# Kernel tuning notes

Measured on AMD Instinct MI355X. Metric: run time of the kernel, lower is better.

Reference implementation:

```python
import jax, jax.numpy as jnp
import numpy as np

B, S, E = 4, 4096, 1024
H = 16
D = E // H  # head_dim = 64


def setup_inputs() -> dict:
    key = jax.random.key(0)
    kx, kk, kq, kv = jax.random.split(key, 4)
    scale = 1.0 / np.sqrt(E)
    return {
        "x": jax.random.normal(kx, (B, S, E), dtype=jnp.float32),
        # torch nn.Linear weight shape: [out_features, in_features] = [D, E]
        "Wk": jax.random.uniform(kk, (D, E), dtype=jnp.float32, minval=-scale, maxval=scale),
        "Wq": jax.random.uniform(kq, (D, E), dtype=jnp.float32, minval=-scale, maxval=scale),
        "Wv": jax.random.uniform(kv, (D, E), dtype=jnp.float32, minval=-scale, maxval=scale),
    }


def reference(x, Wk, Wq, Wv):
    # Projections: x @ W^T  -> [B, S, D]
    k = jnp.einsum('bse,de->bsd', x, Wk)
    q = jnp.einsum('bse,de->bsd', x, Wq)
    v = jnp.einsum('bse,de->bsd', x, Wv)
    # Scaled scores [B, S, S]
    scores = jnp.einsum('bqd,bkd->bqk', q, k) * (D ** -0.5)
    # Causal mask: position q attends to k <= q
    causal = jnp.tril(jnp.ones((S, S), dtype=bool))
    scores = jnp.where(causal, scores, -jnp.inf)
    attn = jax.nn.softmax(scores, axis=-1)
    # dropout omitted (eval mode / attn_pdrop=0)
    out = jnp.einsum('bqk,bkd->bqd', attn, v)
    return out
```

## Files before the change

kernel.cpp:

```cpp
#include <hip/hip_runtime.h>
#include <hip/hip_bf16.h>
#include <stdint.h>

#define BB 4
#define SS 4096
#define EE 1024
#define DD 64

typedef __attribute__((ext_vector_type(8))) short short8;
typedef __attribute__((ext_vector_type(4))) float f32x4;

__device__ inline uint32_t cvtpk(float lo, float hi) {
    uint32_t r;
    asm("v_cvt_pk_bf16_f32 %0, %1, %2" : "=v"(r) : "v"(lo), "v"(hi));
    return r;
}
__device__ inline float bf2f_lo(uint32_t u) {
    union { uint32_t u; float f; } v; v.u = u << 16; return v.f;
}
__device__ inline float bf2f_hi(uint32_t u) {
    union { uint32_t u; float f; } v; v.u = u & 0xFFFF0000u; return v.f;
}

#define GL16(g, l) __builtin_amdgcn_global_load_lds( \
    (const __attribute__((address_space(1))) void*)(g), \
    (__attribute__((address_space(3))) void*)(l), 16, 0, 0)

__global__ __launch_bounds__(256) void wconv_kernel(
    const float* __restrict__ Wq, const float* __restrict__ Wk,
    const float* __restrict__ Wv, ushort* __restrict__ Wb)
{
    int tid = blockIdx.x * 256 + threadIdx.x;
    int sel = tid >> 13;
    int off = (tid & 8191) * 8;
    const float* src = (sel == 0) ? Wq : ((sel == 1) ? Wk : Wv);
    float4 a = *reinterpret_cast<const float4*>(src + off);
    float4 b = *reinterpret_cast<const float4*>(src + off + 4);
    uint4 o;
    o.x = cvtpk(a.x, a.y); o.y = cvtpk(a.z, a.w);
    o.z = cvtpk(b.x, b.y); o.w = cvtpk(b.z, b.w);
    *reinterpret_cast<uint4*>(Wb + (size_t)sel * 65536 + off) = o;
}

__global__ __launch_bounds__(256) void proj_kernel(
    const float* __restrict__ x, const ushort* __restrict__ Wb,
    ushort* __restrict__ q_ws, ushort* __restrict__ k_ws, ushort* __restrict__ vT_ws)
{
    __shared__ __align__(16) char smem[3 * 40960];
    const int t = threadIdx.x;
    const int wid = t >> 6, lane = t & 63, g = lane >> 4, lr = lane & 15;
    const int m0 = blockIdx.x * 64;
    const int NT = EE / 64;

    f32x4 acc[3][4];
#pragma unroll
    for (int ni = 0; ni < 3; ++ni)
#pragma unroll
        for (int mi = 0; mi < 4; ++mi) acc[ni][mi] = (f32x4)(0.0f);

#define PSTAGE(KT, BUFI) do { \
    char* xb_ = smem + (BUFI) * 40960; \
    char* wb_ = xb_ + 16384; \
    int e0_ = (KT) * 64; \
    _Pragma("unroll") \
    for (int i = 0; i < 4; ++i) { \
        int v = i * 256 + t; int row = v >> 4, c = v & 15; \
        GL16(&x[(size_t)(m0 + row) * EE + e0_ + ((c ^ (row & 15)) << 2)], xb_ + v * 16); \
    } \
    _Pragma("unroll") \
    for (int i = 0; i < 6; ++i) { \
        int v = i * 256 + t; int row = v >> 3, u = v & 7; \
        GL16(&Wb[(size_t)row * EE + e0_ + ((u ^ (row & 7)) << 3)], wb_ + v * 16); \
    } \
} while (0)

    PSTAGE(0, 0); PSTAGE(1, 1); PSTAGE(2, 2);

    for (int kt = 0; kt < NT; ++kt) {
        asm volatile("s_waitcnt vmcnt(20)" ::: "memory");
        __builtin_amdgcn_s_barrier();
        __builtin_amdgcn_sched_barrier(0);

        const char* xb = smem + (kt % 3) * 40960;
        const char* wb = xb + 16384;

        short8 af[3][2], bf[4][2];
#pragma unroll
        for (int ni = 0; ni < 3; ++ni) {
            int row = wid * 48 + ni * 16 + lr;
#pragma unroll
            for (int kc = 0; kc < 2; ++kc)
                af[ni][kc] = *reinterpret_cast<const short8*>(
                    wb + row * 128 + (((kc * 4 + g) ^ (row & 7)) << 4));
        }
#pragma unroll
        for (int mi = 0; mi < 4; ++mi) {
            int row = mi * 16 + lr;
#pragma unroll
            for (int kc = 0; kc < 2; ++kc) {
                int s0_ = (kc * 8 + 2 * g) ^ lr;
                int s1_ = (kc * 8 + 2 * g + 1) ^ lr;
                f32x4 lo = *reinterpret_cast<const f32x4*>(xb + row * 256 + s0_ * 16);
                f32x4 hi = *reinterpret_cast<const f32x4*>(xb + row * 256 + s1_ * 16);
                union { short8 s; uint32_t u[4]; } p;
                p.u[0] = cvtpk(lo[0], lo[1]); p.u[1] = cvtpk(lo[2], lo[3]);
                p.u[2] = cvtpk(hi[0], hi[1]); p.u[3] = cvtpk(hi[2], hi[3]);
                bf[mi][kc] = p.s;
            }
        }
#pragma unroll
        for (int ni = 0; ni < 3; ++ni)
#pragma unroll
            for (int mi = 0; mi < 4; ++mi)
#pragma unroll
                for (int kc = 0; kc < 2; ++kc)
                    acc[ni][mi] = __builtin_amdgcn_mfma_f32_16x16x32_bf16(af[ni][kc], bf[mi][kc], acc[ni][mi], 0, 0, 0);

        asm volatile("s_waitcnt lgkmcnt(0)" ::: "memory");
        __builtin_amdgcn_sched_barrier(0);
        __builtin_amdgcn_s_barrier();
        __builtin_amdgcn_sched_barrier(0);

        int nx = (kt + 3 < NT) ? kt + 3 : NT - 1;
        PSTAGE(nx, kt % 3);
    }

    asm volatile("s_waitcnt vmcnt(0)" ::: "memory");

#pragma unroll
    for (int ni = 0; ni < 3; ++ni) {
        int n0 = wid * 48 + ni * 16 + 4 * g;
        int sel = n0 >> 6, d0 = n0 & 63;
#pragma unroll
        for (int mi = 0; mi < 4; ++mi) {
            int m = m0 + mi * 16 + lr;
            int b = m >> 12, s = m & (SS - 1);
            uint2 p;
            p.x = cvtpk(acc[ni][mi][0], acc[ni][mi][1]);
            p.y = cvtpk(acc[ni][mi][2], acc[ni][mi][3]);
            if (sel == 0) {
                *reinterpret_cast<uint2*>(q_ws + ((size_t)b * SS + s) * DD + d0) = p;
            } else if (sel == 1) {
                *reinterpret_cast<uint2*>(k_ws + ((size_t)b * SS + s) * DD + d0) = p;
            } else {
                vT_ws[((size_t)b * DD + d0 + 0) * SS + s] = (ushort)(p.x & 0xFFFF);
                vT_ws[((size_t)b * DD + d0 + 1) * SS + s] = (ushort)(p.x >> 16);
                vT_ws[((size_t)b * DD + d0 + 2) * SS + s] = (ushort)(p.y & 0xFFFF);
                vT_ws[((size_t)b * DD + d0 + 3) * SS + s] = (ushort)(p.y >> 16);
            }
        }
    }
}

__global__ __launch_bounds__(512) void attn_kernel(
    const ushort* __restrict__ q_ws, const ushort* __restrict__ k_ws,
    const ushort* __restrict__ vT_ws, uint32_t* __restrict__ pO32,
    float* __restrict__ pml)
{
    __shared__ __align__(16) char kv_lds[2][32768];
    const int t = threadIdx.x;
    const int wid = t >> 6, lane = t & 63, g = lane >> 4, lr = lane & 15;
    const int bid = blockIdx.x;
    const int f = bid & 3;
    const int b = (bid >> 2) & 3;
    const int qblk = 31 - (bid >> 4);
    const int qb_w = qblk * 128 + wid * 16;

    const ushort* qp = q_ws + ((size_t)b * SS + qb_w + lr) * DD;
    short8 qf0 = *reinterpret_cast<const short8*>(qp + g * 8);
    short8 qf1 = *reinterpret_cast<const short8*>(qp + 32 + g * 8);

    float l_r = 0.0f;
    f32x4 acc[4];
#pragma unroll
    for (int i = 0; i < 4; ++i) acc[i] = (f32x4)(0.0f);

    const float sc = 0.125f * 1.44269504f;
    const float MB = 5.770780164f;
    const int nt = qblk + 1;
    const int nfull = ((qb_w - 127) >> 7) + 1;
    const int cs = (nt + 3) >> 2;
    const int t0 = f * cs;
    const int t1 = min(nt, (f + 1) * cs);
    const ushort* kbase = k_ws + (size_t)b * SS * DD;
    const ushort* vbase = vT_ws + (size_t)b * DD * SS;

    const int s0 = g & 1, hi = g >> 1;
    const int idxA = ((lr + 16 * ((s0 << 1) | hi)) << 2);
    const int idxB = idxA ^ 128;

#define ASTAGE(KT, BUFI) do { \
    char* kb_ = kv_lds[BUFI]; \
    int kv0_ = (KT) * 128; \
    _Pragma("unroll") \
    for (int i = 0; i < 2; ++i) { \
        int v = i * 512 + t; int row = v >> 3, c = v & 7; \
        GL16(kbase + (size_t)(kv0_ + row) * DD + ((c ^ (row & 7)) << 3), kb_ + v * 16); \
    } \
    _Pragma("unroll") \
    for (int i = 0; i < 2; ++i) { \
        int v = i * 512 + t; int row = v >> 4, c = v & 15; \
        GL16(vbase + (size_t)row * SS + kv0_ + ((c ^ ((row & 7) << 1)) << 3), kb_ + 16384 + v * 16); \
    } \
} while (0)

    if (t0 < t1) {
        ASTAGE(t0, 0);
        ASTAGE((t0 + 1 < t1) ? t0 + 1 : t0, 1);

        for (int kt = t0; kt < t1; ++kt) {
            const int cur = (kt - t0) & 1;
            asm volatile("s_waitcnt vmcnt(4)" ::: "memory");
            __builtin_amdgcn_s_barrier();
            __builtin_amdgcn_sched_barrier(0);

            const char* kb = kv_lds[cur];
            const char* vb = kb + 16384;
            const int kv0 = kt * 128;

            f32x4 sfr[8];
            __builtin_amdgcn_s_setprio(1);
#pragma unroll
            for (int nf = 0; nf < 8; ++nf) {
                int row = nf * 16 + lr;
                short8 b0 = *reinterpret_cast<const short8*>(kb + row * 128 + ((g ^ (row & 7)) << 4));
                short8 b1 = *reinterpret_cast<const short8*>(kb + row * 128 + (((4 + g) ^ (row & 7)) << 4));
                f32x4 s_ = (f32x4)(0.0f);
                s_ = __builtin_amdgcn_mfma_f32_16x16x32_bf16(b0, qf0, s_, 0, 0, 0);
                s_ = __builtin_amdgcn_mfma_f32_16x16x32_bf16(b1, qf1, s_, 0, 0, 0);
                sfr[nf] = s_;
            }
            __builtin_amdgcn_s_setprio(0);

            if (kt >= nfull) {
#pragma unroll
                for (int nf = 0; nf < 8; ++nf)
#pragma unroll
                    for (int jr = 0; jr < 4; ++jr)
                        if (kv0 + nf * 16 + 4 * g + jr > qb_w + lr) sfr[nf][jr] = -1e30f;
            }

            float ps = 0.0f;
            uint32_t pk[16];
#pragma unroll
            for (int nf = 0; nf < 8; ++nf) {
                float e0_ = exp2f(fmaf(sfr[nf][0], sc, -MB));
                float e1_ = exp2f(fmaf(sfr[nf][1], sc, -MB));
                float e2_ = exp2f(fmaf(sfr[nf][2], sc, -MB));
                float e3_ = exp2f(fmaf(sfr[nf][3], sc, -MB));
                ps += (e0_ + e1_) + (e2_ + e3_);
                pk[nf * 2 + 0] = cvtpk(e0_, e1_);
                pk[nf * 2 + 1] = cvtpk(e2_, e3_);
            }
            l_r += ps;

            uint32_t pw[4][4];
#pragma unroll
            for (int cc = 0; cc < 4; ++cc) {
                uint32_t r0 = (uint32_t)__builtin_amdgcn_ds_permute(idxA, (int)(s0 ? pk[cc * 4 + 2] : pk[cc * 4 + 0]));
                uint32_t r1 = (uint32_t)__builtin_amdgcn_ds_permute(idxA, (int)(s0 ? pk[cc * 4 + 3] : pk[cc * 4 + 1]));
                uint32_t r2 = (uint32_t)__builtin_amdgcn_ds_permute(idxB, (int)(s0 ? pk[cc * 4 + 0] : pk[cc * 4 + 2]));
                uint32_t r3 = (uint32_t)__builtin_amdgcn_ds_permute(idxB, (int)(s0 ? pk[cc * 4 + 1] : pk[cc * 4 + 3]));
                pw[cc][0] = hi ? r2 : r0;
                pw[cc][1] = hi ? r3 : r1;
                pw[cc][2] = hi ? r0 : r2;
                pw[cc][3] = hi ? r1 : r3;
            }

            __builtin_amdgcn_s_setprio(1);
#pragma unroll
            for (int cc = 0; cc < 4; ++cc) {
                union { uint32_t u[4]; short8 s; } pb;
                pb.u[0] = pw[cc][0]; pb.u[1] = pw[cc][1];
                pb.u[2] = pw[cc][2]; pb.u[3] = pw[cc][3];
#pragma unroll
                for (int df = 0; df < 4; ++df) {
                    int row = df * 16 + lr;
                    short8 vb_ = *reinterpret_cast<const short8*>(
                        vb + row * 256 + (((cc * 4 + g) ^ ((row & 7) << 1)) << 4));
                    acc[df] = __builtin_amdgcn_mfma_f32_16x16x32_bf16(vb_, pb.s, acc[df], 0, 0, 0);
                }
            }
            __builtin_amdgcn_s_setprio(0);

            asm volatile("s_waitcnt lgkmcnt(0)" ::: "memory");
            __builtin_amdgcn_sched_barrier(0);
            __builtin_amdgcn_s_barrier();
            __builtin_amdgcn_sched_barrier(0);

            int nx = (kt + 2 < t1) ? kt + 2 : t1 - 1;
            ASTAGE(nx, cur);
        }
    }
    asm volatile("s_waitcnt vmcnt(0)" ::: "memory");

    l_r += __shfl_xor(l_r, 16);
    l_r += __shfl_xor(l_r, 32);
    const int pidx = ((b * 256 + qblk * 8 + wid) * 4 + f);
    uint32_t* po = pO32 + (size_t)pidx * 512;
#pragma unroll
    for (int df = 0; df < 4; ++df) {
        po[(df * 8 + 2 * g + 0) * 16 + lr] = cvtpk(acc[df][0], acc[df][1]);
        po[(df * 8 + 2 * g + 1) * 16 + lr] = cvtpk(acc[df][2], acc[df][3]);
    }
    if (g == 0) pml[(size_t)pidx * 16 + lr] = l_r;
}

__global__ __launch_bounds__(64) void combine_kernel(
    const uint32_t* __restrict__ pO32, const float* __restrict__ pml,
    float* __restrict__ out)
{
    const int t = threadIdx.x;
    const int q = t & 15, dblk = t >> 4;
    const int grp = blockIdx.x;
    const int b = grp >> 8, qt = grp & 255;
    const int qb = qt * 16;

    float l = 0.0f;
#pragma unroll
    for (int f = 0; f < 4; ++f) l += pml[(size_t)(grp * 4 + f) * 16 + q];

    float o[16];
#pragma unroll
    for (int i = 0; i < 16; ++i) o[i] = 0.0f;
#pragma unroll
    for (int f = 0; f < 4; ++f) {
        const uint32_t* src = pO32 + (size_t)(grp * 4 + f) * 512 + dblk * 128 + q;
#pragma unroll
        for (int r0 = 0; r0 < 8; ++r0) {
            uint32_t u = src[r0 * 16];
            o[2 * r0 + 0] += bf2f_lo(u);
            o[2 * r0 + 1] += bf2f_hi(u);
        }
    }
    float inv = 1.0f / l;
    float* op = out + ((size_t)b * SS + qb + q) * DD + dblk * 16;
#pragma unroll
    for (int i = 0; i < 4; ++i) {
        float4 st;
        st.x = o[4 * i + 0] * inv; st.y = o[4 * i + 1] * inv;
        st.z = o[4 * i + 2] * inv; st.w = o[4 * i + 3] * inv;
        *reinterpret_cast<float4*>(op + 4 * i) = st;
    }
}

extern "C" void kernel_launch(void* const* d_in, const int* in_sizes, int n_in,
                              void* d_out, int out_size, void* d_ws, size_t ws_size,
                              hipStream_t stream) {
    const float* x  = (const float*)d_in[0];
    const float* Wk = (const float*)d_in[1];
    const float* Wq = (const float*)d_in[2];
    const float* Wv = (const float*)d_in[3];
    ushort* q_ws  = (ushort*)d_ws;
    ushort* k_ws  = q_ws + (size_t)BB * SS * DD;
    ushort* vT_ws = k_ws + (size_t)BB * SS * DD;
    ushort* Wb    = vT_ws + (size_t)BB * SS * DD;
    uint32_t* pO32 = (uint32_t*)(Wb + 192 * 1024);
    float* pml     = (float*)(pO32 + (size_t)4096 * 512);
    float* out = (float*)d_out;

    hipLaunchKernelGGL(wconv_kernel, dim3(96), dim3(256), 0, stream, Wq, Wk, Wv, Wb);
    hipLaunchKernelGGL(proj_kernel, dim3(BB * SS / 64), dim3(256), 0, stream,
                       x, Wb, q_ws, k_ws, vT_ws);
    hipLaunchKernelGGL(attn_kernel, dim3(BB * 32 * 4), dim3(512), 0, stream,
                       q_ws, k_ws, vT_ws, pO32, pml);
    hipLaunchKernelGGL(combine_kernel, dim3(BB * SS / 16), dim3(64), 0, stream,
                       pO32, pml, out);
}
```

Baseline: 59.59 us.

## Replace triple-buffered direct-to-LDS loads with register-staged prefetch in projection

The projection GEMM drops its 3-stage global_load_lds pipeline, which kept fp32 x in LDS and converted it to bf16 on every fragment read. Instead, x and W tiles are loaded into registers one iteration ahead, x is converted to bf16 once, and both are written into small single-buffered swizzled LDS tiles. This cuts LDS footprint and redundant conversions, which may allow more resident blocks. The cost is a shallower prefetch depth, two block barriers per iteration and extra register pressure.

```diff
diff --git a/kernel.cpp b/kernel.cpp
--- a/kernel.cpp
+++ b/kernel.cpp
@@ -21,6 +21,8 @@
 __device__ inline float bf2f_hi(uint32_t u) {
     union { uint32_t u; float f; } v; v.u = u & 0xFFFF0000u; return v.f;
 }
+
+#define SWZ16(r, bc) ((bc) ^ (((r) & 7) << 4))
 
 #define GL16(g, l) __builtin_amdgcn_global_load_lds( \
     (const __attribute__((address_space(1))) void*)(g), \
@@ -46,11 +48,11 @@
     const float* __restrict__ x, const ushort* __restrict__ Wb,
     ushort* __restrict__ q_ws, ushort* __restrict__ k_ws, ushort* __restrict__ vT_ws)
 {
-    __shared__ __align__(16) char smem[3 * 40960];
+    __shared__ __align__(16) ushort x_lds[64 * 64];
+    __shared__ __align__(16) ushort w_lds[192 * 64];
     const int t = threadIdx.x;
     const int wid = t >> 6, lane = t & 63, g = lane >> 4, lr = lane & 15;
     const int m0 = blockIdx.x * 64;
-    const int NT = EE / 64;
 
     f32x4 acc[3][4];
 #pragma unroll
@@ -58,74 +60,64 @@
 #pragma unroll
         for (int mi = 0; mi < 4; ++mi) acc[ni][mi] = (f32x4)(0.0f);
 
-#define PSTAGE(KT, BUFI) do { \
-    char* xb_ = smem + (BUFI) * 40960; \
-    char* wb_ = xb_ + 16384; \
-    int e0_ = (KT) * 64; \
+    float4 xr[4];
+    uint4 wr[6];
+
+#define LOADX(E0) do { \
     _Pragma("unroll") \
     for (int i = 0; i < 4; ++i) { \
-        int v = i * 256 + t; int row = v >> 4, c = v & 15; \
-        GL16(&x[(size_t)(m0 + row) * EE + e0_ + ((c ^ (row & 15)) << 2)], xb_ + v * 16); \
+        int idx = i * 256 + t; int row = idx >> 4, c4 = idx & 15; \
+        xr[i] = *reinterpret_cast<const float4*>(&x[(size_t)(m0 + row) * EE + (E0) + c4 * 4]); \
     } \
+} while (0)
+#define LOADW(E0) do { \
     _Pragma("unroll") \
     for (int i = 0; i < 6; ++i) { \
-        int v = i * 256 + t; int row = v >> 3, u = v & 7; \
-        GL16(&Wb[(size_t)row * EE + e0_ + ((u ^ (row & 7)) << 3)], wb_ + v * 16); \
+        int idx = i * 256 + t; int row = idx >> 3, c8 = idx & 7; \
+        wr[i] = *reinterpret_cast<const uint4*>(&Wb[(size_t)row * EE + (E0) + c8 * 8]); \
     } \
 } while (0)
 
-    PSTAGE(0, 0); PSTAGE(1, 1); PSTAGE(2, 2);
-
-    for (int kt = 0; kt < NT; ++kt) {
-        asm volatile("s_waitcnt vmcnt(20)" ::: "memory");
-        __builtin_amdgcn_s_barrier();
-        __builtin_amdgcn_sched_barrier(0);
-
-        const char* xb = smem + (kt % 3) * 40960;
-        const char* wb = xb + 16384;
+    LOADX(0); LOADW(0);
+    for (int e0 = 0; e0 < EE; e0 += 64) {
+#pragma unroll
+        for (int i = 0; i < 4; ++i) {
+            int idx = i * 256 + t; int row = idx >> 4, c4 = idx & 15;
+            uint2 p; p.x = cvtpk(xr[i].x, xr[i].y); p.y = cvtpk(xr[i].z, xr[i].w);
+            *reinterpret_cast<uint2*>((char*)x_lds + row * 128 + SWZ16(row, c4 * 8)) = p;
+        }
+#pragma unroll
+        for (int i = 0; i < 6; ++i) {
+            int idx = i * 256 + t; int row = idx >> 3, c8 = idx & 7;
+            *reinterpret_cast<uint4*>((char*)w_lds + row * 128 + SWZ16(row, c8 * 16)) = wr[i];
+        }
+        __syncthreads();
+        if (e0 + 64 < EE) { LOADX(e0 + 64); LOADW(e0 + 64); }
 
         short8 af[3][2], bf[4][2];
 #pragma unroll
-        for (int ni = 0; ni < 3; ++ni) {
-            int row = wid * 48 + ni * 16 + lr;
-#pragma unroll
-            for (int kc = 0; kc < 2; ++kc)
-                af[ni][kc] = *reinterpret_cast<const short8*>(
-                    wb + row * 128 + (((kc * 4 + g) ^ (row & 7)) << 4));
-        }
-#pragma unroll
-        for (int mi = 0; mi < 4; ++mi) {
-            int row = mi * 16 + lr;
-#pragma unroll
-            for (int kc = 0; kc < 2; ++kc) {
-                int s0_ = (kc * 8 + 2 * g) ^ lr;
-                int s1_ = (kc * 8 + 2 * g + 1) ^ lr;
-                f32x4 lo = *reinterpret_cast<const f32x4*>(xb + row * 256 + s0_ * 16);
-                f32x4 hi = *reinterpret_cast<const f32x4*>(xb + row * 256 + s1_ * 16);
-                union { short8 s; uint32_t u[4]; } p;
-                p.u[0] = cvtpk(lo[0], lo[1]); p.u[1] = cvtpk(lo[2], lo[3]);
-                p.u[2] = cvtpk(hi[0], hi[1]); p.u[3] = cvtpk(hi[2], hi[3]);
-                bf[mi][kc] = p.s;
-            }
-        }
-#pragma unroll
         for (int ni = 0; ni < 3; ++ni)
 #pragma unroll
+            for (int c = 0; c < 2; ++c) {
+                int row = wid * 48 + ni * 16 + lr;
+                af[ni][c] = *reinterpret_cast<const short8*>((const char*)w_lds + row * 128 + SWZ16(row, c * 64 + g * 16));
+            }
+#pragma unroll
+        for (int mi = 0; mi < 4; ++mi)
+#pragma unroll
+            for (int c = 0; c < 2; ++c) {
+                int row = mi * 16 + lr;
+                bf[mi][c] = *reinterpret_cast<const short8*>((const char*)x_lds + row * 128 + SWZ16(row, c * 64 + g * 16));
+            }
+#pragma unroll
+        for (int ni = 0; ni < 3; ++ni)
+#pragma unroll
             for (int mi = 0; mi < 4; ++mi)
 #pragma unroll
-                for (int kc = 0; kc < 2; ++kc)
-                    acc[ni][mi] = __builtin_amdgcn_mfma_f32_16x16x32_bf16(af[ni][kc], bf[mi][kc], acc[ni][mi], 0, 0, 0);
-
-        asm volatile("s_waitcnt lgkmcnt(0)" ::: "memory");
-        __builtin_amdgcn_sched_barrier(0);
-        __builtin_amdgcn_s_barrier();
-        __builtin_amdgcn_sched_barrier(0);
-
-        int nx = (kt + 3 < NT) ? kt + 3 : NT - 1;
-        PSTAGE(nx, kt % 3);
-    }
-
-    asm volatile("s_waitcnt vmcnt(0)" ::: "memory");
+                for (int c = 0; c < 2; ++c)
+                    acc[ni][mi] = __builtin_amdgcn_mfma_f32_16x16x32_bf16(af[ni][c], bf[mi][c], acc[ni][mi], 0, 0, 0);
+        __syncthreads();
+    }
 
 #pragma unroll
     for (int ni = 0; ni < 3; ++ni) {
```

Measured after the change: 75.71 us. 1.27x slower.
